# Kernel optimization log

Hardware: AMD Instinct MI355X
Metric: run time of the kernel (lower is better)

## Reference

```python
import jax, jax.numpy as jnp
import numpy as np

EPS = 1e-5
ROPE_BASE = 10000.0


def _layernorm(x, g, b):
    mu = jnp.mean(x, axis=-1, keepdims=True)
    var = jnp.mean(jnp.square(x - mu), axis=-1, keepdims=True)
    return (x - mu) * jax.lax.rsqrt(var + EPS) * g + b


def _rope(q, k):
    # q, k: (B, T, H, D); rotate interleaved pairs along last dim, positions over T
    T, D = q.shape[1], q.shape[-1]
    half = D // 2
    inv_freq = ROPE_BASE ** (-jnp.arange(half, dtype=jnp.float32) / half)
    ang = jnp.arange(T, dtype=jnp.float32)[:, None] * inv_freq  # (T, half)
    cos = jnp.cos(ang)[None, :, None, :]
    sin = jnp.sin(ang)[None, :, None, :]

    def rot(x):
        xr, xi = x[..., 0::2], x[..., 1::2]
        yr = xr * cos - xi * sin
        yi = xr * sin + xi * cos
        return jnp.stack([yr, yi], axis=-1).reshape(x.shape)

    return rot(q), rot(k)


def setup_inputs() -> dict:
    key = jax.random.key(0)
    ks = jax.random.split(key, 5)
    E, F, B, T = 1024, 4096, 2, 2048
    s = 0.02
    return {
        "x": jax.random.normal(ks[0], (B, T, E), jnp.float32),
        "in_proj_w": jax.random.normal(ks[1], (3 * E, E), jnp.float32) * s,
        "out_proj_w": jax.random.normal(ks[2], (E, E), jnp.float32) * s,
        "ln1_g": jnp.ones((E,), jnp.float32),
        "ln1_b": jnp.zeros((E,), jnp.float32),
        "ln2_g": jnp.ones((E,), jnp.float32),
        "ln2_b": jnp.zeros((E,), jnp.float32),
        "w1": jax.random.normal(ks[3], (F, E), jnp.float32) * s,
        "w2": jax.random.normal(ks[4], (E, F), jnp.float32) * s,
        "context": 256,
    }


def reference(x, in_proj_w, out_proj_w, ln1_g, ln1_b, ln2_g, ln2_b, w1, w2, context):
    B, T, E = x.shape
    H = 16
    D = E // H

    # ---- self-attention block (pre-norm, residual) ----
    h = _layernorm(x, ln1_g, ln1_b)
    proj = h @ in_proj_w.T  # (B, T, 3E)
    qkv = proj.reshape(B, T, 3, H, D)
    q = qkv[:, :, 0]  # (B, T, H, D)
    k = qkv[:, :, 1]
    v = qkv[:, :, 2].transpose(0, 2, 1, 3)  # (B, H, T, D)
    q, k = _rope(q, k)
    q = q.transpose(0, 2, 1, 3)  # (B, H, T, D)
    k = k.transpose(0, 2, 1, 3)

    pos = jnp.arange(T)
    delta = pos[:, None] - pos[None, :]  # (T, T)
    mask = (delta >= 0) & (delta < context)

    scores = jnp.einsum("bhtd,bhsd->bhts", q, k) / jnp.sqrt(jnp.float32(D))
    scores = jnp.where(mask[None, None], scores, jnp.float32(-1e30))
    attn = jax.nn.softmax(scores, axis=-1)
    o = jnp.einsum("bhts,bhsd->bhtd", attn, v)
    o = o.transpose(0, 2, 1, 3).reshape(B, T, E)
    x = x + o @ out_proj_w.T

    # ---- FFN block (pre-norm, residual) ----
    h = _layernorm(x, ln2_g, ln2_b)
    update = jax.nn.gelu(h @ w1.T, approximate=False) @ w2.T
    return x + update
```

## Files before the change

### kernel.cpp

```cpp
#include <hip/hip_runtime.h>
#include <math.h>

#define B_BATCH 2
#define T_SEQ   2048
#define E_DIM   1024
#define H_HEADS 16
#define D_HEAD  64
#define F_DIM   4096
#define M_ROWS  (B_BATCH * T_SEQ)

typedef __attribute__((ext_vector_type(8))) short short8;
typedef __attribute__((ext_vector_type(4))) float floatx4;
typedef __attribute__((ext_vector_type(8))) unsigned short ushortx8;

typedef __attribute__((address_space(1))) const void global_cvoid;
typedef __attribute__((address_space(3))) void lds_void;

__device__ __forceinline__ unsigned short f2bf(float f) {
    unsigned u = __float_as_uint(f);
    u += 0x7fffu + ((u >> 16) & 1u);
    return (unsigned short)(u >> 16);
}
__device__ __forceinline__ float bf2f(unsigned short h) {
    return __uint_as_float(((unsigned)h) << 16);
}

__device__ __forceinline__ float waveReduceSum(float v) {
#pragma unroll
    for (int off = 32; off > 0; off >>= 1) v += __shfl_xor(v, off, 64);
    return v;
}

__global__ __launch_bounds__(256) void cvt_kernel(const float* __restrict__ in,
                                                  unsigned short* __restrict__ out,
                                                  int n) {
    const int i = (blockIdx.x * 256 + threadIdx.x) * 4;
    if (i >= n) return;
    float4 v = *(const float4*)(in + i);
    ushort4 o;
    o.x = f2bf(v.x); o.y = f2bf(v.y); o.z = f2bf(v.z); o.w = f2bf(v.w);
    *(ushort4*)(out + i) = o;
}

__global__ __launch_bounds__(256) void reduce4_kernel(const float* __restrict__ p,
                                                      float* __restrict__ out, int n) {
    const int i = (blockIdx.x * 256 + threadIdx.x) * 4;
    if (i >= n) return;
    float4 a  = *(const float4*)(out + i);
    float4 b0 = *(const float4*)(p + i);
    float4 b1 = *(const float4*)(p + (size_t)n + i);
    float4 b2 = *(const float4*)(p + 2 * (size_t)n + i);
    float4 b3 = *(const float4*)(p + 3 * (size_t)n + i);
    a.x += b0.x + b1.x + b2.x + b3.x;
    a.y += b0.y + b1.y + b2.y + b3.y;
    a.z += b0.z + b1.z + b2.z + b3.z;
    a.w += b0.w + b1.w + b2.w + b3.w;
    *(float4*)(out + i) = a;
}

__global__ __launch_bounds__(256) void rope_tab_kernel(float* __restrict__ tab) {
    const int idx = blockIdx.x * 256 + threadIdx.x;
    const int pos = idx >> 5, i = idx & 31;
    const float invf = powf(10000.0f, -(float)i / 32.0f);
    const float ang = (float)pos * invf;
    tab[idx * 2]     = cosf(ang);
    tab[idx * 2 + 1] = sinf(ang);
}

__global__ __launch_bounds__(256) void ln_kernel(const float* __restrict__ x,
                                                 const float* __restrict__ g,
                                                 const float* __restrict__ b,
                                                 unsigned short* __restrict__ out) {
    const int row = blockIdx.x;
    const float* xr = x + (size_t)row * E_DIM;
    float4 v = ((const float4*)xr)[threadIdx.x];
    float s  = v.x + v.y + v.z + v.w;
    float sq = v.x * v.x + v.y * v.y + v.z * v.z + v.w * v.w;

    __shared__ float red[8];
    float ws_ = waveReduceSum(s);
    float wq  = waveReduceSum(sq);
    int wid = threadIdx.x >> 6;
    if ((threadIdx.x & 63) == 0) { red[wid] = ws_; red[wid + 4] = wq; }
    __syncthreads();
    float ts = red[0] + red[1] + red[2] + red[3];
    float tq = red[4] + red[5] + red[6] + red[7];
    float mean = ts * (1.0f / E_DIM);
    float var  = tq * (1.0f / E_DIM) - mean * mean;
    float inv  = rsqrtf(var + 1e-5f);

    float4 gv = ((const float4*)g)[threadIdx.x];
    float4 bv = ((const float4*)b)[threadIdx.x];
    ushort4 o;
    o.x = f2bf((v.x - mean) * inv * gv.x + bv.x);
    o.y = f2bf((v.y - mean) * inv * gv.y + bv.y);
    o.z = f2bf((v.z - mean) * inv * gv.z + bv.z);
    o.w = f2bf((v.w - mean) * inv * gv.w + bv.w);
    ((ushort4*)(out + (size_t)row * E_DIM))[threadIdx.x] = o;
}

template <int EPI>
__global__ __launch_bounds__(256) void gemm_bf16(const unsigned short* __restrict__ A,
                                                 const unsigned short* __restrict__ Wt,
                                                 const float* __restrict__ R,
                                                 float* __restrict__ Cf,
                                                 unsigned short* __restrict__ Cb,
                                                 int M, int N, int K) {
    __shared__ unsigned short As[128 * 64];
    __shared__ unsigned short Bs[128 * 64];
    const int tid  = threadIdx.x;
    const int wave = tid >> 6, lane = tid & 63;
    const int wm   = wave >> 1, wn = wave & 1;
    const int quad = lane >> 4, l16 = lane & 15;
    const int m0 = blockIdx.y * 128, n0 = blockIdx.x * 128;
    const int Kc   = K / gridDim.z;
    const int kbeg = blockIdx.z * Kc;

    const int row_rel = lane >> 3;
    const int ch      = lane & 7;

    const floatx4 z = {0.0f, 0.0f, 0.0f, 0.0f};
    floatx4 acc[4][4];
#pragma unroll
    for (int i = 0; i < 4; ++i)
#pragma unroll
        for (int j = 0; j < 4; ++j) acc[i][j] = z;

    for (int k0 = kbeg; k0 < kbeg + Kc; k0 += 64) {
        __syncthreads();
#pragma unroll
        for (int i = 0; i < 4; ++i) {
            const int chunk = wave * 4 + i;
            const int grow  = chunk * 8 + row_rel;
            const int lch   = ch ^ (grow & 7);
            const unsigned short* ga = A  + (size_t)(m0 + grow) * K + k0 + lch * 8;
            const unsigned short* gb = Wt + (size_t)(n0 + grow) * K + k0 + lch * 8;
            __builtin_amdgcn_global_load_lds((global_cvoid*)ga,
                                             (lds_void*)(As + chunk * 512), 16, 0, 0);
            __builtin_amdgcn_global_load_lds((global_cvoid*)gb,
                                             (lds_void*)(Bs + chunk * 512), 16, 0, 0);
        }
        __syncthreads();

#pragma unroll
        for (int ks = 0; ks < 2; ++ks) {
            short8 af[4], bfr[4];
#pragma unroll
            for (int mt = 0; mt < 4; ++mt) {
                const int r = wm * 64 + mt * 16 + l16;
                const int p = (ks * 4 + quad) ^ (r & 7);
                af[mt] = *(const short8*)(As + r * 64 + p * 8);
            }
#pragma unroll
            for (int nt = 0; nt < 4; ++nt) {
                const int r = wn * 64 + nt * 16 + l16;
                const int p = (ks * 4 + quad) ^ (r & 7);
                bfr[nt] = *(const short8*)(Bs + r * 64 + p * 8);
            }
#pragma unroll
            for (int mt = 0; mt < 4; ++mt)
#pragma unroll
                for (int nt = 0; nt < 4; ++nt)
                    acc[mt][nt] = __builtin_amdgcn_mfma_f32_16x16x32_bf16(
                        af[mt], bfr[nt], acc[mt][nt], 0, 0, 0);
        }
    }

#pragma unroll
    for (int mt = 0; mt < 4; ++mt) {
        const int rb = m0 + wm * 64 + mt * 16 + quad * 4;
#pragma unroll
        for (int nt = 0; nt < 4; ++nt) {
            const int col = n0 + wn * 64 + nt * 16 + l16;
#pragma unroll
            for (int r = 0; r < 4; ++r) {
                const size_t idx = (size_t)(rb + r) * N + col;
                const float v = acc[mt][nt][r];
                if (EPI == 1) {
                    Cf[idx] = v + R[idx];
                } else {
                    Cf[idx] = v;
                }
            }
        }
    }
}

template <int EPI>
__global__ __launch_bounds__(512, 2) void gemm256_bf16(const unsigned short* __restrict__ A,
                                                       const unsigned short* __restrict__ Wt,
                                                       float* __restrict__ Cf,
                                                       unsigned short* __restrict__ Cb,
                                                       int M, int N, int K) {
    __shared__ __align__(16) unsigned short Ls[3 * 16384];

    const int tid  = threadIdx.x;
    const int wave = tid >> 6, lane = tid & 63;
    const int wm   = wave >> 2, wn = wave & 3;
    const int quad = lane >> 4, l16 = lane & 15;

    int bid = blockIdx.y * gridDim.x + blockIdx.x;
    const int cpx = (gridDim.x * gridDim.y) >> 3;
    bid = (bid & 7) * cpx + (bid >> 3);
    const int bx = bid % gridDim.x, by = bid / gridDim.x;
    const int m0 = by * 256, n0 = bx * 256;

    const int Kc   = K / gridDim.z;
    const int kbeg = blockIdx.z * Kc;
    const int NT   = Kc >> 5;

    const int rr = lane >> 2;
    const int ch = lane & 3;

    const floatx4 z = {0.0f, 0.0f, 0.0f, 0.0f};
    floatx4 acc[8][4];
#pragma unroll
    for (int i = 0; i < 8; ++i)
#pragma unroll
        for (int j = 0; j < 4; ++j) acc[i][j] = z;

    auto STAGE = [&](int t, int bi) {
        const int k0 = kbeg + t * 32;
#pragma unroll
        for (int i = 0; i < 2; ++i) {
            const int g    = wave * 2 + i;
            const int grow = g * 16 + rr;
            const int sch  = (ch ^ ((grow >> 1) & 3)) * 8;
            const unsigned short* ga = A  + (size_t)(m0 + grow) * K + k0 + sch;
            const unsigned short* gb = Wt + (size_t)(n0 + grow) * K + k0 + sch;
            unsigned short* la = Ls + bi * 16384 + g * 512;
            __builtin_amdgcn_global_load_lds((global_cvoid*)ga, (lds_void*)la,        16, 0, 0);
            __builtin_amdgcn_global_load_lds((global_cvoid*)gb, (lds_void*)(la + 8192), 16, 0, 0);
        }
    };

    STAGE(0, 0);
    STAGE(1, 1);
    asm volatile("s_waitcnt vmcnt(4)" ::: "memory");
    __builtin_amdgcn_s_barrier();
    __builtin_amdgcn_sched_barrier(0);

    int bi = 0, pb = 2;
    for (int t = 0; t < NT; ++t) {
        const bool pf = (t + 2 < NT);
        if (pf) STAGE(t + 2, pb);

        const unsigned short* Ab = Ls + bi * 16384;
        const unsigned short* Bb = Ab + 8192;
        short8 af[8], bfr[4];
#pragma unroll
        for (int mt = 0; mt < 8; ++mt) {
            const int r = wm * 128 + mt * 16 + l16;
            af[mt] = *(const short8*)(Ab + r * 32 + ((quad ^ ((r >> 1) & 3)) * 8));
        }
#pragma unroll
        for (int nt = 0; nt < 4; ++nt) {
            const int r = wn * 64 + nt * 16 + l16;
            bfr[nt] = *(const short8*)(Bb + r * 32 + ((quad ^ ((r >> 1) & 3)) * 8));
        }

        __builtin_amdgcn_s_setprio(1);
#pragma unroll
        for (int mt = 0; mt < 8; ++mt)
#pragma unroll
            for (int nt = 0; nt < 4; ++nt)
                acc[mt][nt] = __builtin_amdgcn_mfma_f32_16x16x32_bf16(
                    af[mt], bfr[nt], acc[mt][nt], 0, 0, 0);
        __builtin_amdgcn_s_setprio(0);

        if (pf) asm volatile("s_waitcnt vmcnt(4)" ::: "memory");
        else    asm volatile("s_waitcnt vmcnt(0)" ::: "memory");
        __builtin_amdgcn_s_barrier();
        __builtin_amdgcn_sched_barrier(0);

        bi = (bi == 2) ? 0 : bi + 1;
        pb = (pb == 2) ? 0 : pb + 1;
    }

    const size_t zoff = (size_t)blockIdx.z * M * N;
#pragma unroll
    for (int mt = 0; mt < 8; ++mt) {
        const int rb = m0 + wm * 128 + mt * 16 + quad * 4;
#pragma unroll
        for (int nt = 0; nt < 4; ++nt) {
            const int col = n0 + wn * 64 + nt * 16 + l16;
#pragma unroll
            for (int r = 0; r < 4; ++r) {
                const size_t idx = (size_t)(rb + r) * N + col;
                const float v = acc[mt][nt][r];
                if (EPI == 2) {
                    Cb[idx] = f2bf(0.5f * v * (1.0f + erff(v * 0.70710678118654752f)));
                } else if (EPI == 4) {
                    Cb[idx] = f2bf(v);
                } else {
                    Cf[zoff + idx] = v;
                }
            }
        }
    }
}

__global__ __launch_bounds__(256) void vtrans_kernel(const unsigned short* __restrict__ proj,
                                                     unsigned short* __restrict__ vt) {
    __shared__ unsigned short L[64 * 72];
    const int bh = blockIdx.y, b = bh >> 4, h = bh & 15;
    const int st = blockIdx.x * 64;
    const int tid = threadIdx.x;
    {
        const int srel = tid >> 2, d16 = (tid & 3) * 16;
        const unsigned short* src =
            proj + (size_t)(b * T_SEQ + st + srel) * (3 * E_DIM) + 2 * E_DIM + h * 64 + d16;
        *(short8*)(L + srel * 72 + d16)     = *(const short8*)(src);
        *(short8*)(L + srel * 72 + d16 + 8) = *(const short8*)(src + 8);
    }
    __syncthreads();
    {
        const int d = tid >> 2, s16 = (tid & 3) * 16;
        short8 o0, o1;
#pragma unroll
        for (int j = 0; j < 8; ++j) {
            o0[j] = (short)L[(s16 + j) * 72 + d];
            o1[j] = (short)L[(s16 + 8 + j) * 72 + d];
        }
        unsigned short* dst = vt + (size_t)(bh * 64 + d) * T_SEQ + st + s16;
        *(short8*)dst       = o0;
        *(short8*)(dst + 8) = o1;
    }
}

__device__ __forceinline__ void rope16(ushortx8 x0, ushortx8 x1, const float* tp,
                                       short8& y0, short8& y1) {
#pragma unroll
    for (int j = 0; j < 4; ++j) {
        const float c = tp[2 * j], s = tp[2 * j + 1];
        const float xr = bf2f(x0[2 * j]), xi = bf2f(x0[2 * j + 1]);
        y0[2 * j]     = (short)f2bf(xr * c - xi * s);
        y0[2 * j + 1] = (short)f2bf(xr * s + xi * c);
    }
#pragma unroll
    for (int j = 0; j < 4; ++j) {
        const float c = tp[8 + 2 * j], s = tp[8 + 2 * j + 1];
        const float xr = bf2f(x1[2 * j]), xi = bf2f(x1[2 * j + 1]);
        y1[2 * j]     = (short)f2bf(xr * c - xi * s);
        y1[2 * j + 1] = (short)f2bf(xr * s + xi * c);
    }
}

__global__ __launch_bounds__(256) void attn_kernel(const unsigned short* __restrict__ proj,
                                                   const unsigned short* __restrict__ vt,
                                                   const float* __restrict__ tab,
                                                   const int* __restrict__ ctxp,
                                                   unsigned short* __restrict__ o) {
    __shared__ unsigned short Qs[64 * 64];
    __shared__ unsigned short Ks[64 * 64];
    __shared__ unsigned short Vs[64 * 64];
    __shared__ unsigned short Ps[4][16 * 64];

    const int ctx = ctxp[0];
    const int tid = threadIdx.x;
    const int wave = tid >> 6, lane = tid & 63;
    const int quad = lane >> 4, l16 = lane & 15;
    const int bh = blockIdx.y, b = bh >> 4, h = bh & 15;
    const int t0 = blockIdx.x * 64;

    {
        const int r = tid >> 2, d16 = (tid & 3) * 16;
        const int pos = t0 + r;
        const unsigned short* src =
            proj + (size_t)(b * T_SEQ + pos) * (3 * E_DIM) + h * 64 + d16;
        ushortx8 x0 = *(const ushortx8*)src;
        ushortx8 x1 = *(const ushortx8*)(src + 8);
        const float* tp = tab + ((size_t)pos * 32 + (d16 >> 1)) * 2;
        short8 y0, y1;
        rope16(x0, x1, tp, y0, y1);
        const int c0 = (tid & 3) * 2;
        *(short8*)(Qs + r * 64 + ((c0)     ^ (r & 7)) * 8) = y0;
        *(short8*)(Qs + r * 64 + ((c0 + 1) ^ (r & 7)) * 8) = y1;
    }

    int first = t0 - (ctx - 1);
    if (first < 0) first = 0;
    const int first_base = first & ~63;

    float m[4] = {-1e30f, -1e30f, -1e30f, -1e30f};
    float l[4] = {0.0f, 0.0f, 0.0f, 0.0f};
    const floatx4 z = {0.0f, 0.0f, 0.0f, 0.0f};
    floatx4 accO[4] = {z, z, z, z};

    const int q_row0 = t0 + wave * 16 + quad * 4;

    for (int s_base = first_base; s_base <= t0; s_base += 64) {
        __syncthreads();
        {
            const int r = tid >> 2, d16 = (tid & 3) * 16;
            const int pos = s_base + r;
            const unsigned short* src =
                proj + (size_t)(b * T_SEQ + pos) * (3 * E_DIM) + E_DIM + h * 64 + d16;
            ushortx8 x0 = *(const ushortx8*)src;
            ushortx8 x1 = *(const ushortx8*)(src + 8);
            const float* tp = tab + ((size_t)pos * 32 + (d16 >> 1)) * 2;
            short8 y0, y1;
            rope16(x0, x1, tp, y0, y1);
            const int c0 = (tid & 3) * 2;
            *(short8*)(Ks + r * 64 + ((c0)     ^ (r & 7)) * 8) = y0;
            *(short8*)(Ks + r * 64 + ((c0 + 1) ^ (r & 7)) * 8) = y1;
        }
#pragma unroll
        for (int i = 0; i < 2; ++i) {
            const int chunk = (wave * 2 + i) * 64 + lane;
            const int d = chunk >> 3, c = chunk & 7;
            const unsigned short* gsrc =
                vt + (size_t)(bh * 64 + d) * T_SEQ + s_base + ((c ^ (d & 7)) * 8);
            __builtin_amdgcn_global_load_lds((global_cvoid*)gsrc,
                                             (lds_void*)(Vs + (wave * 2 + i) * 512),
                                             16, 0, 0);
        }
        __syncthreads();

        floatx4 accS[4] = {z, z, z, z};
#pragma unroll
        for (int ks = 0; ks < 2; ++ks) {
            const int qrow = wave * 16 + l16;
            short8 aq = *(const short8*)(Qs + qrow * 64 + (((ks * 4 + quad) ^ (qrow & 7)) * 8));
#pragma unroll
            for (int nt = 0; nt < 4; ++nt) {
                const int kro = nt * 16 + l16;
                short8 bk = *(const short8*)(Ks + kro * 64 + (((ks * 4 + quad) ^ (kro & 7)) * 8));
                accS[nt] = __builtin_amdgcn_mfma_f32_16x16x32_bf16(aq, bk, accS[nt], 0, 0, 0);
            }
        }

        float p[4][4];
        float alpha[4];
#pragma unroll
        for (int r = 0; r < 4; ++r) {
            const int qa = q_row0 + r;
            float sv[4];
            float vmax = -1e30f;
#pragma unroll
            for (int nt = 0; nt < 4; ++nt) {
                const int sa = s_base + nt * 16 + l16;
                const int dd = qa - sa;
                const bool ok = (unsigned)dd < (unsigned)ctx;
                const float s = ok ? accS[nt][r] * 0.125f : -1e30f;
                sv[nt] = s;
                vmax = fmaxf(vmax, s);
            }
            vmax = fmaxf(vmax, __shfl_xor(vmax, 1));
            vmax = fmaxf(vmax, __shfl_xor(vmax, 2));
            vmax = fmaxf(vmax, __shfl_xor(vmax, 4));
            vmax = fmaxf(vmax, __shfl_xor(vmax, 8));
            const float mn = fmaxf(m[r], vmax);
            alpha[r] = __expf(m[r] - mn);
            float ps = 0.0f;
#pragma unroll
            for (int nt = 0; nt < 4; ++nt) {
                const float pe = (sv[nt] > -0.5e30f) ? __expf(sv[nt] - mn) : 0.0f;
                p[nt][r] = pe;
                ps += pe;
            }
            ps += __shfl_xor(ps, 1);
            ps += __shfl_xor(ps, 2);
            ps += __shfl_xor(ps, 4);
            ps += __shfl_xor(ps, 8);
            l[r] = l[r] * alpha[r] + ps;
            m[r] = mn;
        }

#pragma unroll
        for (int nt = 0; nt < 4; ++nt) {
#pragma unroll
            for (int r = 0; r < 4; ++r) {
                const int row = quad * 4 + r;
                const int col = nt * 16 + l16;
                Ps[wave][row * 64 + (((col >> 3) ^ (row & 7)) * 8) + (col & 7)] =
                    f2bf(p[nt][r]);
            }
        }
#pragma unroll
        for (int nt = 0; nt < 4; ++nt)
#pragma unroll
            for (int r = 0; r < 4; ++r) accO[nt][r] *= alpha[r];

#pragma unroll
        for (int ks = 0; ks < 2; ++ks) {
            short8 ap = *(const short8*)(&Ps[wave][l16 * 64 + (((ks * 4 + quad) ^ (l16 & 7)) * 8)]);
#pragma unroll
            for (int nt = 0; nt < 4; ++nt) {
                const int dr = nt * 16 + l16;
                short8 bv = *(const short8*)(Vs + dr * 64 + (((ks * 4 + quad) ^ (dr & 7)) * 8));
                accO[nt] = __builtin_amdgcn_mfma_f32_16x16x32_bf16(ap, bv, accO[nt], 0, 0, 0);
            }
        }
    }

    float inv[4];
#pragma unroll
    for (int r = 0; r < 4; ++r) inv[r] = 1.0f / l[r];
#pragma unroll
    for (int nt = 0; nt < 4; ++nt) {
#pragma unroll
        for (int r = 0; r < 4; ++r) {
            const int t = q_row0 + r;
            o[(size_t)(b * T_SEQ + t) * E_DIM + h * 64 + nt * 16 + l16] =
                f2bf(accO[nt][r] * inv[r]);
        }
    }
}

extern "C" void kernel_launch(void* const* d_in, const int* in_sizes, int n_in,
                              void* d_out, int out_size, void* d_ws, size_t ws_size,
                              hipStream_t stream) {
    const float* x          = (const float*)d_in[0];
    const float* in_proj_w  = (const float*)d_in[1];
    const float* out_proj_w = (const float*)d_in[2];
    const float* ln1_g      = (const float*)d_in[3];
    const float* ln1_b      = (const float*)d_in[4];
    const float* ln2_g      = (const float*)d_in[5];
    const float* ln2_b      = (const float*)d_in[6];
    const float* w1         = (const float*)d_in[7];
    const float* w2         = (const float*)d_in[8];
    const int*   ctx        = (const int*)d_in[9];
    float* out = (float*)d_out;
    float* ws  = (float*)d_ws;

    const size_t MEG = 1024u * 1024u;
    unsigned short* u = (unsigned short*)ws;
    unsigned short* wqkv_b = u;
    unsigned short* wout_b = u + 3 * MEG;
    unsigned short* w1_b   = u + 4 * MEG;
    unsigned short* h_b    = u + 8 * MEG;
    unsigned short* obuf_b = u + 12 * MEG;
    unsigned short* proj_b = u + 16 * MEG;
    unsigned short* vt_b   = u + 28 * MEG;
    unsigned short* mid_b  = u + 32 * MEG;
    unsigned short* w2_b   = u + 48 * MEG;
    float* tab  = ws + 26 * MEG;
    float* part = ws;

    cvt_kernel<<<3 * E_DIM * E_DIM / 1024, 256, 0, stream>>>(in_proj_w, wqkv_b, 3 * E_DIM * E_DIM);
    cvt_kernel<<<E_DIM * E_DIM / 1024, 256, 0, stream>>>(out_proj_w, wout_b, E_DIM * E_DIM);
    cvt_kernel<<<F_DIM * E_DIM / 1024, 256, 0, stream>>>(w1, w1_b, F_DIM * E_DIM);
    cvt_kernel<<<E_DIM * F_DIM / 1024, 256, 0, stream>>>(w2, w2_b, E_DIM * F_DIM);
    rope_tab_kernel<<<T_SEQ * 32 / 256, 256, 0, stream>>>(tab);

    ln_kernel<<<M_ROWS, 256, 0, stream>>>(x, ln1_g, ln1_b, h_b);
    gemm256_bf16<4><<<dim3(3 * E_DIM / 256, M_ROWS / 256), 512, 0, stream>>>(
        h_b, wqkv_b, nullptr, proj_b, M_ROWS, 3 * E_DIM, E_DIM);
    vtrans_kernel<<<dim3(T_SEQ / 64, B_BATCH * H_HEADS), 256, 0, stream>>>(proj_b, vt_b);
    attn_kernel<<<dim3(T_SEQ / 64, B_BATCH * H_HEADS), 256, 0, stream>>>(
        proj_b, vt_b, tab, ctx, obuf_b);
    gemm_bf16<1><<<dim3(E_DIM / 128, M_ROWS / 128), 256, 0, stream>>>(
        obuf_b, wout_b, x, out, nullptr, M_ROWS, E_DIM, E_DIM);
    ln_kernel<<<M_ROWS, 256, 0, stream>>>(out, ln2_g, ln2_b, h_b);
    gemm256_bf16<2><<<dim3(F_DIM / 256, M_ROWS / 256), 512, 0, stream>>>(
        h_b, w1_b, nullptr, mid_b, M_ROWS, F_DIM, E_DIM);
    gemm256_bf16<5><<<dim3(E_DIM / 256, M_ROWS / 256, 4), 512, 0, stream>>>(
        mid_b, w2_b, part, nullptr, M_ROWS, E_DIM, F_DIM);
    reduce4_kernel<<<M_ROWS * E_DIM / 1024, 256, 0, stream>>>(
        part, out, M_ROWS * E_DIM);
}
```

Baseline: 347.2 us.

## Deepen GEMM LDS pipeline to four stages with inline-asm reads and fast GELU

The 256x256 bf16 GEMM moves from a 3-buffer to a 4-buffer LDS ring that prefetches three tiles ahead. The main loop is unrolled by four with constant buffer offsets and raw ds_read_b128 inline asm, which removes per-iteration index arithmetic. The erff-based GELU epilogue is replaced by an Abramowitz-Stegun polynomial erf approximation using rcp and exp. LDS use grows to 128KB per block, which may limit occupancy under the (512,2) launch bounds. The tail assumes NT is a multiple of four and at least 4, and the GELU is slightly less accurate.

```diff
diff --git a/kernel.cpp b/kernel.cpp
--- a/kernel.cpp
+++ b/kernel.cpp
@@ -23,6 +23,24 @@
 }
 __device__ __forceinline__ float bf2f(unsigned short h) {
     return __uint_as_float(((unsigned)h) << 16);
+}
+
+__device__ __forceinline__ unsigned lds_lo(const void* p) {
+    return (unsigned)(unsigned long long)p;
+}
+
+__device__ __forceinline__ float gelu_f(float v) {
+    const float x = fabsf(v) * 0.70710678118654752f;
+    const float t = __builtin_amdgcn_rcpf(__builtin_fmaf(0.3275911f, x, 1.0f));
+    float p = __builtin_fmaf(1.061405429f, t, -1.453152027f);
+    p = __builtin_fmaf(p, t, 1.421413741f);
+    p = __builtin_fmaf(p, t, -0.284496736f);
+    p = __builtin_fmaf(p, t, 0.254829592f);
+    p *= t;
+    const float e = __expf(-x * x);
+    float er = __builtin_fmaf(-p, e, 1.0f);
+    er = copysignf(er, v);
+    return 0.5f * v * (1.0f + er);
 }
 
 __device__ __forceinline__ float waveReduceSum(float v) {
@@ -192,7 +210,7 @@
                                                        float* __restrict__ Cf,
                                                        unsigned short* __restrict__ Cb,
                                                        int M, int N, int K) {
-    __shared__ __align__(16) unsigned short Ls[3 * 16384];
+    __shared__ __align__(16) unsigned short Ls[4 * 16384];
 
     const int tid  = threadIdx.x;
     const int wave = tid >> 6, lane = tid & 63;
@@ -234,48 +252,60 @@
         }
     };
 
+    const unsigned swz = (unsigned)(quad ^ ((l16 >> 1) & 3));
+    const unsigned aA = lds_lo(Ls) + (unsigned)(wm * 128 + l16) * 64u + swz * 16u;
+    const unsigned aB = lds_lo(Ls) + 16384u + (unsigned)(wn * 64 + l16) * 64u + swz * 16u;
+
+#define GSTEP(T, C, PD, DOPF, WSTR, DOBAR)                                     \
+    do {                                                                       \
+        if (DOPF) STAGE((T) + 3, (PD));                                        \
+        const unsigned aAc = aA + (C) * 32768u;                                \
+        const unsigned aBc = aB + (C) * 32768u;                                \
+        short8 af[8], bfr[4];                                                  \
+        _Pragma("unroll")                                                      \
+        for (int mt = 0; mt < 8; ++mt)                                         \
+            asm volatile("ds_read_b128 %0, %1"                                 \
+                         : "=v"(af[mt]) : "v"(aAc + mt * 1024u));              \
+        _Pragma("unroll")                                                      \
+        for (int nt = 0; nt < 4; ++nt)                                         \
+            asm volatile("ds_read_b128 %0, %1"                                 \
+                         : "=v"(bfr[nt]) : "v"(aBc + nt * 1024u));             \
+        asm volatile("s_waitcnt lgkmcnt(0)" ::: "memory");                     \
+        __builtin_amdgcn_sched_barrier(0);                                     \
+        __builtin_amdgcn_s_setprio(1);                                         \
+        _Pragma("unroll")                                                      \
+        for (int mt = 0; mt < 8; ++mt)                                         \
+            _Pragma("unroll")                                                  \
+            for (int nt = 0; nt < 4; ++nt)                                     \
+                acc[mt][nt] = __builtin_amdgcn_mfma_f32_16x16x32_bf16(         \
+                    af[mt], bfr[nt], acc[mt][nt], 0, 0, 0);                    \
+        __builtin_amdgcn_s_setprio(0);                                         \
+        if (DOBAR) {                                                           \
+            asm volatile("s_waitcnt " WSTR ::: "memory");                      \
+            __builtin_amdgcn_s_barrier();                                      \
+            __builtin_amdgcn_sched_barrier(0);                                 \
+        }                                                                      \
+    } while (0)
+
     STAGE(0, 0);
     STAGE(1, 1);
-    asm volatile("s_waitcnt vmcnt(4)" ::: "memory");
+    STAGE(2, 2);
+    asm volatile("s_waitcnt vmcnt(8)" ::: "memory");
     __builtin_amdgcn_s_barrier();
     __builtin_amdgcn_sched_barrier(0);
 
-    int bi = 0, pb = 2;
-    for (int t = 0; t < NT; ++t) {
-        const bool pf = (t + 2 < NT);
-        if (pf) STAGE(t + 2, pb);
-
-        const unsigned short* Ab = Ls + bi * 16384;
-        const unsigned short* Bb = Ab + 8192;
-        short8 af[8], bfr[4];
-#pragma unroll
-        for (int mt = 0; mt < 8; ++mt) {
-            const int r = wm * 128 + mt * 16 + l16;
-            af[mt] = *(const short8*)(Ab + r * 32 + ((quad ^ ((r >> 1) & 3)) * 8));
-        }
-#pragma unroll
-        for (int nt = 0; nt < 4; ++nt) {
-            const int r = wn * 64 + nt * 16 + l16;
-            bfr[nt] = *(const short8*)(Bb + r * 32 + ((quad ^ ((r >> 1) & 3)) * 8));
-        }
-
-        __builtin_amdgcn_s_setprio(1);
-#pragma unroll
-        for (int mt = 0; mt < 8; ++mt)
-#pragma unroll
-            for (int nt = 0; nt < 4; ++nt)
-                acc[mt][nt] = __builtin_amdgcn_mfma_f32_16x16x32_bf16(
-                    af[mt], bfr[nt], acc[mt][nt], 0, 0, 0);
-        __builtin_amdgcn_s_setprio(0);
-
-        if (pf) asm volatile("s_waitcnt vmcnt(4)" ::: "memory");
-        else    asm volatile("s_waitcnt vmcnt(0)" ::: "memory");
-        __builtin_amdgcn_s_barrier();
-        __builtin_amdgcn_sched_barrier(0);
-
-        bi = (bi == 2) ? 0 : bi + 1;
-        pb = (pb == 2) ? 0 : pb + 1;
-    }
+    int t = 0;
+    for (; t + 4 < NT; t += 4) {
+        GSTEP(t + 0, 0, 3, true, "vmcnt(8)", true);
+        GSTEP(t + 1, 1, 0, true, "vmcnt(8)", true);
+        GSTEP(t + 2, 2, 1, true, "vmcnt(8)", true);
+        GSTEP(t + 3, 3, 2, true, "vmcnt(8)", true);
+    }
+    GSTEP(t + 0, 0, 3, true,  "vmcnt(8)", true);
+    GSTEP(t + 1, 1, 0, false, "vmcnt(4)", true);
+    GSTEP(t + 2, 2, 1, false, "vmcnt(0)", true);
+    GSTEP(t + 3, 3, 2, false, "vmcnt(0)", false);
+#undef GSTEP
 
     const size_t zoff = (size_t)blockIdx.z * M * N;
 #pragma unroll
@@ -289,7 +319,7 @@
                 const size_t idx = (size_t)(rb + r) * N + col;
                 const float v = acc[mt][nt][r];
                 if (EPI == 2) {
-                    Cb[idx] = f2bf(0.5f * v * (1.0f + erff(v * 0.70710678118654752f)));
+                    Cb[idx] = f2bf(gelu_f(v));
                 } else if (EPI == 4) {
                     Cb[idx] = f2bf(v);
                 } else {
```

New measurement: 325.5 us. 6.2% less time.
